# Performance work log

Measured on AMD Instinct MI355X. Metric: run time of the kernel, lower is better.

The kernel has to match this reference:

```python
import jax, jax.numpy as jnp
import numpy as np

D = 512      # d_model
H = 8        # n_heads
DK = D // H  # head dim
DFF = 4 * D  # d_ff
E = 3        # encoder layers
PRED = 256   # pred_len
C_OUT = 64


def _ln(x, g, b):
    m = jnp.mean(x, axis=-1, keepdims=True)
    v = jnp.var(x, axis=-1, keepdims=True)
    return (x - m) / jnp.sqrt(v + 1e-5) * g + b


def _attn(q_in, kv_in, Wq, bq, Wk, bk, Wv, bv, Wo, bo, causal):
    B, L, _ = q_in.shape
    S = kv_in.shape[1]
    q = (q_in @ Wq + bq).reshape(B, L, H, DK)
    k = (kv_in @ Wk + bk).reshape(B, S, H, DK)
    v = (kv_in @ Wv + bv).reshape(B, S, H, DK)
    scores = jnp.einsum('blhe,bshe->bhls', q, k)  # [B,H,L,S]
    if causal:
        mask = jnp.triu(jnp.ones((L, S), dtype=bool), k=1)
        scores = jnp.where(mask, -jnp.inf, scores)
    scale = 1.0 / jnp.sqrt(jnp.asarray(DK, scores.dtype))
    A = jax.nn.softmax(scores * scale, axis=-1)
    out = jnp.einsum('bhls,bshd->blhd', A, v).reshape(B, L, H * DK)
    return out @ Wo + bo


def _gelu(x):
    return jax.nn.gelu(x, approximate=False)  # torch F.gelu is exact erf


def setup_inputs() -> dict:
    ks = iter(jax.random.split(jax.random.key(0), 80))
    r = lambda *s: jax.random.normal(next(ks), s, jnp.float32) * 0.02
    inp = {}
    inp['x_dec'] = jax.random.normal(next(ks), (8, 512, D), jnp.float32)
    inp['x_enc'] = jax.random.normal(next(ks), (8, 1024, D), jnp.float32)
    # encoder params, stacked over layers
    for nm in ['Wq', 'Wk', 'Wv', 'Wo']:
        inp[f'enc_{nm}'] = r(E, D, D)
        inp[f'enc_b{nm[1].lower()}'] = r(E, D)
    inp['enc_W1'] = r(E, D, DFF); inp['enc_b1'] = r(E, DFF)
    inp['enc_W2'] = r(E, DFF, D); inp['enc_b2'] = r(E, D)
    inp['enc_g1'] = jnp.ones((E, D)); inp['enc_beta1'] = jnp.zeros((E, D))
    inp['enc_g2'] = jnp.ones((E, D)); inp['enc_beta2'] = jnp.zeros((E, D))
    inp['enc_ng'] = jnp.ones((D,)); inp['enc_nbeta'] = jnp.zeros((D,))
    # decoder (single layer) params
    for p in ['s', 'c']:
        for nm in ['Wq', 'Wk', 'Wv', 'Wo']:
            inp[f'dec_{p}{nm}'] = r(D, D)
            inp[f'dec_{p}b{nm[1].lower()}'] = r(D)
    inp['dec_W1'] = r(D, DFF); inp['dec_b1'] = r(DFF)
    inp['dec_W2'] = r(DFF, D); inp['dec_b2'] = r(D)
    inp['dec_g1'] = jnp.ones((D,)); inp['dec_beta1'] = jnp.zeros((D,))
    inp['dec_g2'] = jnp.ones((D,)); inp['dec_beta2'] = jnp.zeros((D,))
    inp['dec_g3'] = jnp.ones((D,)); inp['dec_beta3'] = jnp.zeros((D,))
    inp['dec_ng'] = jnp.ones((D,)); inp['dec_nbeta'] = jnp.zeros((D,))
    inp['proj_W'] = r(D, C_OUT); inp['proj_b'] = r(C_OUT)
    return inp


def reference(x_dec, x_enc,
              enc_Wq, enc_bq, enc_Wk, enc_bk, enc_Wv, enc_bv, enc_Wo, enc_bo,
              enc_W1, enc_b1, enc_W2, enc_b2,
              enc_g1, enc_beta1, enc_g2, enc_beta2, enc_ng, enc_nbeta,
              dec_sWq, dec_sbq, dec_sWk, dec_sbk, dec_sWv, dec_sbv, dec_sWo, dec_sbo,
              dec_cWq, dec_cbq, dec_cWk, dec_cbk, dec_cWv, dec_cbv, dec_cWo, dec_cbo,
              dec_W1, dec_b1, dec_W2, dec_b2,
              dec_g1, dec_beta1, dec_g2, dec_beta2, dec_g3, dec_beta3,
              dec_ng, dec_nbeta, proj_W, proj_b):
    # ----- encoder (non-causal self-attn, eval mode: dropout = identity) -----
    x = x_enc
    for l in range(E):
        a = _attn(x, x, enc_Wq[l], enc_bq[l], enc_Wk[l], enc_bk[l],
                  enc_Wv[l], enc_bv[l], enc_Wo[l], enc_bo[l], causal=False)
        x = _ln(x + a, enc_g1[l], enc_beta1[l])
        y = _gelu(x @ enc_W1[l] + enc_b1[l]) @ enc_W2[l] + enc_b2[l]
        x = _ln(x + y, enc_g2[l], enc_beta2[l])
    enc_out = _ln(x, enc_ng, enc_nbeta)
    # ----- decoder (causal self-attn + cross-attn) -----
    x = x_dec
    a = _attn(x, x, dec_sWq, dec_sbq, dec_sWk, dec_sbk,
              dec_sWv, dec_sbv, dec_sWo, dec_sbo, causal=True)
    x = _ln(x + a, dec_g1, dec_beta1)
    a = _attn(x, enc_out, dec_cWq, dec_cbq, dec_cWk, dec_cbk,
              dec_cWv, dec_cbv, dec_cWo, dec_cbo, causal=False)
    x = _ln(x + a, dec_g2, dec_beta2)
    y = _gelu(x @ dec_W1 + dec_b1) @ dec_W2 + dec_b2
    x = _ln(x + y, dec_g3, dec_beta3)
    x = _ln(x, dec_ng, dec_nbeta)
    out = x @ proj_W + proj_b
    return out[:, -PRED:, :]
```

## Files before the change

kernel.cpp:

```cpp
#include <hip/hip_runtime.h>
#include <cstddef>

typedef __bf16 bf16;
typedef __bf16 bf16x8 __attribute__((ext_vector_type(8)));
typedef float f32x4 __attribute__((ext_vector_type(4)));

#define D 512
#define DFF 2048
#define MFMA __builtin_amdgcn_mfma_f32_16x16x32_bf16

__device__ __forceinline__ float load_any(const void* p, size_t i, int f) {
  return f ? ((const float*)p)[i] : (float)((const bf16*)p)[i];
}

__global__ void detect_dtype(const unsigned* __restrict__ x, int* flag) {
  __shared__ int cnt;
  if (threadIdx.x == 0) cnt = 0;
  __syncthreads();
  int local = 0;
  for (int i = threadIdx.x; i < 32768; i += 256) {
    unsigned e = (x[i] >> 7) & 0xFFu;
    if (e >= 160u) local++;
  }
  atomicAdd(&cnt, local);
  __syncthreads();
  if (threadIdx.x == 0) *flag = (cnt > 100) ? 1 : 0;
}

__global__ __launch_bounds__(256)
void conv_to_bf16(const void* __restrict__ src, bf16* __restrict__ dst, int n,
                  const int* __restrict__ flag) {
  const int f = *flag;
  for (int i = blockIdx.x * 256 + threadIdx.x; i < n; i += gridDim.x * 256)
    dst[i] = (bf16)load_any(src, i, f);
}

struct CDesc { const void* src; unsigned long long off; bf16* dst; int n; int pad; };
struct CPack { CDesc d[40]; };
__global__ __launch_bounds__(256)
void conv_batch(CPack P, const int* __restrict__ flag) {
  const CDesc& c = P.d[blockIdx.z];
  const int f = *flag;
  for (int i = blockIdx.x * 256 + threadIdx.x; i < c.n; i += gridDim.x * 256)
    c.dst[i] = (bf16)load_any(c.src, c.off + i, f);
}

struct TDesc { const void* src; unsigned long long off; bf16* dst; };
struct TPack { TDesc d[20]; };
__global__ __launch_bounds__(256)
void transpose_b(TPack P, int Kd, int Nd, const int* __restrict__ flag) {
  __shared__ bf16 tile[64][65];
  const TDesc& t = P.d[blockIdx.z];
  const int f = *flag;
  int tx = threadIdx.x & 63, ty = threadIdx.x >> 6;
  int nb = blockIdx.x * 64, kb = blockIdx.y * 64;
  #pragma unroll
  for (int r = ty; r < 64; r += 4)
    tile[r][tx] = (bf16)load_any(t.src, t.off + (size_t)(kb + r) * Nd + nb + tx, f);
  __syncthreads();
  #pragma unroll
  for (int r = ty; r < 64; r += 4)
    t.dst[(size_t)(nb + r) * Kd + kb + tx] = tile[tx][r];
}

__global__ __launch_bounds__(256)
void prep_kv(const bf16* __restrict__ K, const bf16* __restrict__ V,
             bf16* __restrict__ Kf, bf16* __restrict__ Vf, int S)
{
  __shared__ bf16 tile[64][72];
  const int kt = blockIdx.x, h = blockIdx.y, b = blockIdx.z;
  const int t = threadIdx.x;
  const int r = t >> 2, g = t & 3;
  const size_t srcrow = ((size_t)(b * S + kt * 64 + r)) * D + h * 64 + g * 16;
  const size_t bh = (size_t)(b * 8 + h);
  const size_t tbase = (bh * (S >> 6) + kt) * 4096;

  bf16x8 k0 = *(const bf16x8*)(K + srcrow);
  bf16x8 k1 = *(const bf16x8*)(K + srcrow + 8);
  const int nt = r >> 4, m15 = r & 15;
  const int c = g >> 1, qq = (g & 1) * 2;
  *(bf16x8*)(Kf + tbase + (((nt * 2 + c) * 64) + qq * 16 + m15) * 8)       = k0;
  *(bf16x8*)(Kf + tbase + (((nt * 2 + c) * 64) + (qq + 1) * 16 + m15) * 8) = k1;

  bf16x8 v0 = *(const bf16x8*)(V + srcrow);
  bf16x8 v1 = *(const bf16x8*)(V + srcrow + 8);
  #pragma unroll
  for (int u = 0; u < 8; u++) {
    tile[g * 16 + u][r]     = v0[u];
    tile[g * 16 + 8 + u][r] = v1[u];
  }
  __syncthreads();
  #pragma unroll
  for (int s = 0; s < 2; s++) {
    int i = t * 2 + s;
    int lane = i & 63, ntc = i >> 6;
    int vq = lane >> 4, vm = lane & 15;
    int vnt = ntc >> 1, vc = ntc & 1;
    bf16x8 o = *(const bf16x8*)(&tile[vnt * 16 + vm][vc * 32 + vq * 8]);
    *(bf16x8*)(Vf + tbase + (size_t)i * 8) = o;
  }
}

__device__ __forceinline__ void gload_lds16(const bf16* g, bf16* l) {
  __builtin_amdgcn_global_load_lds((const __attribute__((address_space(1))) void*)g,
                                   (__attribute__((address_space(3))) void*)l,
                                   16, 0, 0);
}

__device__ __forceinline__ void swizzle_bm_bn(int& bm, int& bn) {
  int lin = blockIdx.y * gridDim.x + blockIdx.x;
  if ((gridDim.y & 7) == 0) {
    int xcd = lin & 7, j = lin >> 3;
    bn = j % gridDim.x;
    bm = xcd + 8 * (j / gridDim.x);
  } else {
    bn = blockIdx.x; bm = blockIdx.y;
  }
}

__global__ __launch_bounds__(256, 2)
void gemm_bt(const bf16* __restrict__ A, const bf16* __restrict__ BT,
             const bf16* __restrict__ bias, bf16* __restrict__ C,
             int M, int N, int K, int act)
{
  __shared__ bf16 As[128 * 32];
  __shared__ bf16 Bs[128 * 32];
  const int tid = threadIdx.x;
  int bm, bn; swizzle_bm_bn(bm, bn);
  const int wid = tid >> 6, lane = tid & 63;
  const int wm = (wid >> 1) << 6, wn = (wid & 1) << 6;
  const int l15 = lane & 15, q = lane >> 4;

  f32x4 acc[4][4] = {};

  const bf16* ag = A + (size_t)(bm * 128 + (tid >> 2)) * K + (tid & 3) * 8;
  const bf16* bg = BT + (size_t)(bn * 128 + (tid >> 2)) * K + (tid & 3) * 8;
  const size_t rstep = (size_t)64 * K;
  bf16* asl = As + tid * 8;
  bf16* bsl = Bs + tid * 8;

  for (int k0 = 0; k0 < K; k0 += 32) {
    __syncthreads();
    gload_lds16(ag + k0,          asl);
    gload_lds16(ag + k0 + rstep,  asl + 256 * 8);
    gload_lds16(bg + k0,          bsl);
    gload_lds16(bg + k0 + rstep,  bsl + 256 * 8);
    __syncthreads();

    bf16x8 af[4], bq[4];
    #pragma unroll
    for (int i = 0; i < 4; i++)
      af[i] = *(const bf16x8*)(As + (wm + i * 16 + l15) * 32 + q * 8);
    #pragma unroll
    for (int j = 0; j < 4; j++)
      bq[j] = *(const bf16x8*)(Bs + (wn + j * 16 + l15) * 32 + q * 8);
    #pragma unroll
    for (int i = 0; i < 4; i++)
      #pragma unroll
      for (int j = 0; j < 4; j++)
        acc[i][j] = MFMA(af[i], bq[j], acc[i][j], 0, 0, 0);
  }

  #pragma unroll
  for (int j = 0; j < 4; j++) {
    int gcol = bn * 128 + wn + j * 16 + l15;
    float bv = (float)bias[gcol];
    #pragma unroll
    for (int i = 0; i < 4; i++) {
      int grow = bm * 128 + wm + i * 16 + q * 4;
      #pragma unroll
      for (int r = 0; r < 4; r++) {
        float v = acc[i][j][r] + bv;
        if (act == 1) v = 0.5f * v * (1.0f + erff(v * 0.70710678118654752f));
        C[(size_t)(grow + r) * N + gcol] = (bf16)v;
      }
    }
  }
}

__global__ __launch_bounds__(256, 2)
void gemm_ks(const bf16* __restrict__ A, const bf16* __restrict__ BT,
             const bf16* __restrict__ bias, bf16* __restrict__ P0,
             bf16* __restrict__ P1, int M, int N, int K)
{
  __shared__ bf16 As[128 * 32];
  __shared__ bf16 Bs[128 * 32];
  const int tid = threadIdx.x;
  int bm, bnl; swizzle_bm_bn(bm, bnl);
  const int bn = bnl >> 1, split = bnl & 1;
  const int Kh = K >> 1, kbase = split * Kh;
  const int wid = tid >> 6, lane = tid & 63;
  const int wm = (wid >> 1) << 6, wn = (wid & 1) << 6;
  const int l15 = lane & 15, q = lane >> 4;

  f32x4 acc[4][4] = {};

  const bf16* ag = A + (size_t)(bm * 128 + (tid >> 2)) * K + kbase + (tid & 3) * 8;
  const bf16* bg = BT + (size_t)(bn * 128 + (tid >> 2)) * K + kbase + (tid & 3) * 8;
  const size_t rstep = (size_t)64 * K;
  bf16* asl = As + tid * 8;
  bf16* bsl = Bs + tid * 8;

  for (int k0 = 0; k0 < Kh; k0 += 32) {
    __syncthreads();
    gload_lds16(ag + k0,          asl);
    gload_lds16(ag + k0 + rstep,  asl + 256 * 8);
    gload_lds16(bg + k0,          bsl);
    gload_lds16(bg + k0 + rstep,  bsl + 256 * 8);
    __syncthreads();

    bf16x8 af[4], bq[4];
    #pragma unroll
    for (int i = 0; i < 4; i++)
      af[i] = *(const bf16x8*)(As + (wm + i * 16 + l15) * 32 + q * 8);
    #pragma unroll
    for (int j = 0; j < 4; j++)
      bq[j] = *(const bf16x8*)(Bs + (wn + j * 16 + l15) * 32 + q * 8);
    #pragma unroll
    for (int i = 0; i < 4; i++)
      #pragma unroll
      for (int j = 0; j < 4; j++)
        acc[i][j] = MFMA(af[i], bq[j], acc[i][j], 0, 0, 0);
  }

  bf16* Cp = split ? P1 : P0;
  #pragma unroll
  for (int j = 0; j < 4; j++) {
    int gcol = bn * 128 + wn + j * 16 + l15;
    float bv = split ? 0.0f : (float)bias[gcol];
    #pragma unroll
    for (int i = 0; i < 4; i++) {
      int grow = bm * 128 + wm + i * 16 + q * 4;
      #pragma unroll
      for (int r = 0; r < 4; r++)
        Cp[(size_t)(grow + r) * 512 + gcol] = (bf16)(acc[i][j][r] + bv);
    }
  }
}

__global__ __launch_bounds__(256, 2)
void gemm_seg(const bf16* __restrict__ A, const bf16* __restrict__ BT,
              const bf16* __restrict__ bias,
              bf16* __restrict__ O0, bf16* __restrict__ O1, bf16* __restrict__ O2,
              int M, int K)
{
  __shared__ bf16 As[128 * 32];
  __shared__ bf16 Bs[128 * 32];
  const int tid = threadIdx.x;
  int bm, bn; swizzle_bm_bn(bm, bn);
  const int wid = tid >> 6, lane = tid & 63;
  const int wm = (wid >> 1) << 6, wn = (wid & 1) << 6;
  const int l15 = lane & 15, q = lane >> 4;

  f32x4 acc[4][4] = {};

  const bf16* ag = A + (size_t)(bm * 128 + (tid >> 2)) * K + (tid & 3) * 8;
  const bf16* bg = BT + (size_t)(bn * 128 + (tid >> 2)) * K + (tid & 3) * 8;
  const size_t rstep = (size_t)64 * K;
  bf16* asl = As + tid * 8;
  bf16* bsl = Bs + tid * 8;

  for (int k0 = 0; k0 < K; k0 += 32) {
    __syncthreads();
    gload_lds16(ag + k0,          asl);
    gload_lds16(ag + k0 + rstep,  asl + 256 * 8);
    gload_lds16(bg + k0,          bsl);
    gload_lds16(bg + k0 + rstep,  bsl + 256 * 8);
    __syncthreads();

    bf16x8 af[4], bq[4];
    #pragma unroll
    for (int i = 0; i < 4; i++)
      af[i] = *(const bf16x8*)(As + (wm + i * 16 + l15) * 32 + q * 8);
    #pragma unroll
    for (int j = 0; j < 4; j++)
      bq[j] = *(const bf16x8*)(Bs + (wn + j * 16 + l15) * 32 + q * 8);
    #pragma unroll
    for (int i = 0; i < 4; i++)
      #pragma unroll
      for (int j = 0; j < 4; j++)
        acc[i][j] = MFMA(af[i], bq[j], acc[i][j], 0, 0, 0);
  }

  const int seg = (bn * 128) >> 9;
  bf16* Cp = (seg == 0) ? O0 : ((seg == 1) ? O1 : O2);
  const int colb = seg << 9;

  #pragma unroll
  for (int j = 0; j < 4; j++) {
    int gcol = bn * 128 + wn + j * 16 + l15;
    float bv = (float)bias[gcol];
    int lcol = gcol - colb;
    #pragma unroll
    for (int i = 0; i < 4; i++) {
      int grow = bm * 128 + wm + i * 16 + q * 4;
      #pragma unroll
      for (int r = 0; r < 4; r++)
        Cp[(size_t)(grow + r) * 512 + lcol] = (bf16)(acc[i][j][r] + bv);
    }
  }
}

__global__ __launch_bounds__(256, 2)
void flash_attn(const bf16* __restrict__ Q, const bf16* __restrict__ Kf,
                const bf16* __restrict__ Vf, bf16* __restrict__ O,
                int L, int S, int causal)
{
  __shared__ bf16 PL[4][32 * 72];
  const int tid = threadIdx.x, wid = tid >> 6, lane = tid & 63;
  const int m15 = lane & 15, q = lane >> 4;
  const int b = blockIdx.z, h = blockIdx.y;
  const int wq = blockIdx.x * 128 + wid * 32;

  bf16x8 aq[2][2];
  #pragma unroll
  for (int qh = 0; qh < 2; qh++) {
    const bf16* qp = Q + ((size_t)(b * L + wq + qh * 16 + m15)) * D + h * 64 + q * 8;
    aq[qh][0] = *(const bf16x8*)(qp);
    aq[qh][1] = *(const bf16x8*)(qp + 32);
  }
  const size_t bh = (size_t)(b * 8 + h);
  const bf16* kfb = Kf + bh * ((size_t)S * 64);
  const bf16* vfb = Vf + bh * ((size_t)S * 64);

  f32x4 acco[2][4] = {};
  float ls[2][4] = {};

  const int ktmax = causal ? ((wq + 95) >> 6) : (S >> 6);

  bf16x8 kf[4][2];
  #pragma unroll
  for (int nt = 0; nt < 4; nt++)
    #pragma unroll
    for (int c = 0; c < 2; c++)
      kf[nt][c] = *(const bf16x8*)(kfb + ((nt * 2 + c) * 64 + lane) * 8);

  bf16* pl = &PL[wid][0];

  for (int kt = 0; kt < ktmax; kt++) {
    bf16x8 vf[4][2];
    const bf16* vc = vfb + (size_t)kt * 4096;
    #pragma unroll
    for (int nt = 0; nt < 4; nt++)
      #pragma unroll
      for (int c = 0; c < 2; c++)
        vf[nt][c] = *(const bf16x8*)(vc + ((nt * 2 + c) * 64 + lane) * 8);

    f32x4 sc[2][4];
    #pragma unroll
    for (int qh = 0; qh < 2; qh++)
      #pragma unroll
      for (int nt = 0; nt < 4; nt++) {
        f32x4 z = {};
        z = MFMA(aq[qh][0], kf[nt][0], z, 0, 0, 0);
        z = MFMA(aq[qh][1], kf[nt][1], z, 0, 0, 0);
        sc[qh][nt] = z;
      }

    {
      const int knext = (kt + 1 < ktmax) ? kt + 1 : kt;
      const bf16* kc = kfb + (size_t)knext * 4096;
      #pragma unroll
      for (int nt = 0; nt < 4; nt++)
        #pragma unroll
        for (int c = 0; c < 2; c++)
          kf[nt][c] = *(const bf16x8*)(kc + ((nt * 2 + c) * 64 + lane) * 8);
    }

    const bool mask = causal && (kt == ktmax - 1);
    #pragma unroll
    for (int qh = 0; qh < 2; qh++)
      #pragma unroll
      for (int nt = 0; nt < 4; nt++)
        #pragma unroll
        for (int r = 0; r < 4; r++) {
          float s = sc[qh][nt][r] * 0.125f;
          if (mask) {
            int kg = kt * 64 + nt * 16 + m15;
            int qg = wq + qh * 16 + q * 4 + r;
            if (kg > qg) s = -1e30f;
          }
          float p = __expf(s);
          ls[qh][r] += p;
          pl[(qh * 16 + q * 4 + r) * 72 + nt * 16 + m15] = (bf16)p;
        }

    #pragma unroll
    for (int qh = 0; qh < 2; qh++) {
      bf16x8 pa0 = *(const bf16x8*)(pl + (qh * 16 + m15) * 72 + q * 8);
      bf16x8 pa1 = *(const bf16x8*)(pl + (qh * 16 + m15) * 72 + 32 + q * 8);
      #pragma unroll
      for (int nt = 0; nt < 4; nt++) {
        acco[qh][nt] = MFMA(pa0, vf[nt][0], acco[qh][nt], 0, 0, 0);
        acco[qh][nt] = MFMA(pa1, vf[nt][1], acco[qh][nt], 0, 0, 0);
      }
    }
  }

  #pragma unroll
  for (int qh = 0; qh < 2; qh++)
    #pragma unroll
    for (int r = 0; r < 4; r++) {
      float v = ls[qh][r];
      v += __shfl_xor(v, 1); v += __shfl_xor(v, 2);
      v += __shfl_xor(v, 4); v += __shfl_xor(v, 8);
      ls[qh][r] = 1.0f / v;
    }

  #pragma unroll
  for (int qh = 0; qh < 2; qh++)
    #pragma unroll
    for (int nt = 0; nt < 4; nt++)
      #pragma unroll
      for (int r = 0; r < 4; r++)
        O[((size_t)(b * L + wq + qh * 16 + q * 4 + r)) * D + h * 64 + nt * 16 + m15] =
            (bf16)(acco[qh][nt][r] * ls[qh][r]);
}

__global__ __launch_bounds__(256)
void add_ln(const bf16* __restrict__ X0, const bf16* __restrict__ X1,
            const bf16* __restrict__ R,
            const bf16* __restrict__ g, const bf16* __restrict__ be,
            bf16* __restrict__ Y, int hasR)
{
  __shared__ float red[4];
  const int row = blockIdx.x, tid = threadIdx.x;
  const bf16* x = X0 + (size_t)row * D;
  float v0 = (float)x[tid], v1 = (float)x[tid + 256];
  if (X1 != nullptr) {
    const bf16* p = X1 + (size_t)row * D;
    v0 += (float)p[tid]; v1 += (float)p[tid + 256];
  }
  if (hasR) {
    const bf16* r = R + (size_t)row * D;
    v0 += (float)r[tid]; v1 += (float)r[tid + 256];
  }
  float s = v0 + v1;
  #pragma unroll
  for (int o = 32; o > 0; o >>= 1) s += __shfl_down(s, o);
  if ((tid & 63) == 0) red[tid >> 6] = s;
  __syncthreads();
  const float mean = (red[0] + red[1] + red[2] + red[3]) * (1.0f / 512.0f);
  __syncthreads();
  const float d0 = v0 - mean, d1 = v1 - mean;
  float sq = d0 * d0 + d1 * d1;
  #pragma unroll
  for (int o = 32; o > 0; o >>= 1) sq += __shfl_down(sq, o);
  if ((tid & 63) == 0) red[tid >> 6] = sq;
  __syncthreads();
  const float var = (red[0] + red[1] + red[2] + red[3]) * (1.0f / 512.0f);
  const float rstd = rsqrtf(var + 1e-5f);
  bf16* y = Y + (size_t)row * D;
  y[tid]       = (bf16)(d0 * rstd * (float)g[tid]       + (float)be[tid]);
  y[tid + 256] = (bf16)(d1 * rstd * (float)g[tid + 256] + (float)be[tid + 256]);
}

__global__ __launch_bounds__(256)
void proj_out(const bf16* __restrict__ X, const bf16* __restrict__ Wp,
              const bf16* __restrict__ bp, void* __restrict__ out,
              const int* __restrict__ flag)
{
  __shared__ float part[4][64];
  const int rb = blockIdx.x;
  const int b = rb >> 8, t = rb & 255;
  const int tid = threadIdx.x;
  const bf16* x = X + ((size_t)(b * 512 + 256 + t)) * D;
  const int c = tid & 63, seg = tid >> 6;
  float acc = 0.f;
  for (int k = seg * 128; k < seg * 128 + 128; k++)
    acc += (float)x[k] * (float)Wp[(size_t)k * 64 + c];
  part[seg][c] = acc;
  __syncthreads();
  if (tid < 64) {
    float v = part[0][tid] + part[1][tid] + part[2][tid] + part[3][tid] + (float)bp[tid];
    size_t idx = (size_t)rb * 64 + tid;
    if (*flag) ((float*)out)[idx] = v;
    else       ((bf16*)out)[idx] = (bf16)v;
  }
}

extern "C" void kernel_launch(void* const* d_in, const int* in_sizes, int n_in,
                              void* d_out, int out_size, void* d_ws, size_t ws_size,
                              hipStream_t stream)
{
  (void)in_sizes; (void)n_in; (void)out_size; (void)ws_size;

  char* wsb = (char*)d_ws;
  int* flag = (int*)wsb;
  bf16* w = (bf16*)(wsb + 256);
  size_t off = 0;
  auto alloc = [&](size_t n) { bf16* p = w + off; off += n; return p; };

  bf16* eQKVT = alloc(3 * (size_t)1536 * D);
  bf16* eWoT  = alloc(3 * (size_t)D * D);
  bf16* eW1T  = alloc(3 * (size_t)D * DFF);
  bf16* eW2T  = alloc(3 * (size_t)D * DFF);
  bf16* dQKVT = alloc((size_t)1536 * D);
  bf16* sWoT  = alloc((size_t)D * D);
  bf16* cWqT  = alloc((size_t)D * D);
  bf16* cKVT  = alloc((size_t)1024 * D);
  bf16* cWoT  = alloc((size_t)D * D);
  bf16* dW1T  = alloc((size_t)D * DFF);
  bf16* dW2T  = alloc((size_t)D * DFF);
  bf16* pW    = alloc((size_t)D * 64);
  bf16* e_qkvb  = alloc(3 * 1536);
  bf16* d_sqkvb = alloc(1536);
  bf16* d_ckvb  = alloc(1024);
  bf16* c_ebo = alloc(3 * D);
  bf16* c_eb1 = alloc(3 * DFF); bf16* c_eb2 = alloc(3 * D);
  bf16* c_eg1 = alloc(3 * D);   bf16* c_ebe1 = alloc(3 * D);
  bf16* c_eg2 = alloc(3 * D);   bf16* c_ebe2 = alloc(3 * D);
  bf16* c_eng = alloc(D);       bf16* c_enb = alloc(D);
  bf16* c_dsbo = alloc(D);
  bf16* c_dcbq = alloc(D);      bf16* c_dcbo = alloc(D);
  bf16* c_db1 = alloc(DFF);     bf16* c_db2 = alloc(D);
  bf16* c_dg1 = alloc(D);  bf16* c_dbe1 = alloc(D);
  bf16* c_dg2 = alloc(D);  bf16* c_dbe2 = alloc(D);
  bf16* c_dg3 = alloc(D);  bf16* c_dbe3 = alloc(D);
  bf16* c_dng = alloc(D);  bf16* c_dnb = alloc(D);
  bf16* c_pb  = alloc(64);
  bf16* xe   = alloc((size_t)8192 * D);
  bf16* enco = alloc((size_t)8192 * D);
  bf16* xd0  = alloc((size_t)4096 * D);
  bf16* xd   = alloc((size_t)4096 * D);
  bf16* qb   = alloc((size_t)8192 * D);
  bf16* kb   = alloc((size_t)8192 * D);
  bf16* vb   = alloc((size_t)8192 * D);
  bf16* t0   = alloc((size_t)8192 * D);
  bf16* t1   = alloc((size_t)8192 * D);
  bf16* mid  = qb;

  const dim3 tb(256);

  detect_dtype<<<dim3(1), tb, 0, stream>>>((const unsigned*)d_in[1], flag);

  conv_to_bf16<<<dim3(1024), tb, 0, stream>>>(d_in[1], xe, 8 * 1024 * D, flag);
  conv_to_bf16<<<dim3(1024), tb, 0, stream>>>(d_in[0], xd0, 8 * 512 * D, flag);

  {
    CPack P{};
    int n = 0;
    auto add = [&](int idx, unsigned long long o, bf16* dst, int cnt) {
      P.d[n++] = {d_in[idx], o, dst, cnt, 0};
    };
    add(9, 0, c_ebo, 1536);
    add(11, 0, c_eb1, 6144);  add(13, 0, c_eb2, 1536);
    add(14, 0, c_eg1, 1536);  add(15, 0, c_ebe1, 1536);
    add(16, 0, c_eg2, 1536);  add(17, 0, c_ebe2, 1536);
    add(18, 0, c_eng, 512);   add(19, 0, c_enb, 512);
    add(27, 0, c_dsbo, 512);
    add(29, 0, c_dcbq, 512);  add(35, 0, c_dcbo, 512);
    add(37, 0, c_db1, 2048);  add(39, 0, c_db2, 512);
    add(40, 0, c_dg1, 512);   add(41, 0, c_dbe1, 512);
    add(42, 0, c_dg2, 512);   add(43, 0, c_dbe2, 512);
    add(44, 0, c_dg3, 512);   add(45, 0, c_dbe3, 512);
    add(46, 0, c_dng, 512);   add(47, 0, c_dnb, 512);
    add(48, 0, pW, D * 64);   add(49, 0, c_pb, 64);
    for (int l = 0; l < 3; l++) {
      add(3, (unsigned long long)l * D, e_qkvb + l * 1536, 512);
      add(5, (unsigned long long)l * D, e_qkvb + l * 1536 + 512, 512);
      add(7, (unsigned long long)l * D, e_qkvb + l * 1536 + 1024, 512);
    }
    add(21, 0, d_sqkvb, 512); add(23, 0, d_sqkvb + 512, 512); add(25, 0, d_sqkvb + 1024, 512);
    add(31, 0, d_ckvb, 512);  add(33, 0, d_ckvb + 512, 512);
    conv_batch<<<dim3(24, 1, n), tb, 0, stream>>>(P, flag);
  }

  {
    TPack P{};
    int n = 0;
    for (int l = 0; l < 3; l++) {
      unsigned long long wo = (unsigned long long)l * D * D;
      bf16* dst = eQKVT + (size_t)l * 1536 * D;
      P.d[n++] = {d_in[2], wo, dst};
      P.d[n++] = {d_in[4], wo, dst + 512 * D};
      P.d[n++] = {d_in[6], wo, dst + 1024 * D};
      P.d[n++] = {d_in[8], wo, eWoT + wo};
    }
    P.d[n++] = {d_in[20], 0, dQKVT};
    P.d[n++] = {d_in[22], 0, dQKVT + 512 * D};
    P.d[n++] = {d_in[24], 0, dQKVT + 1024 * D};
    P.d[n++] = {d_in[26], 0, sWoT};
    P.d[n++] = {d_in[28], 0, cWqT};
    P.d[n++] = {d_in[30], 0, cKVT};
    P.d[n++] = {d_in[32], 0, cKVT + 512 * D};
    P.d[n++] = {d_in[34], 0, cWoT};
    transpose_b<<<dim3(8, 8, n), tb, 0, stream>>>(P, D, D, flag);
  }
  {
    TPack P{};
    for (int l = 0; l < 3; l++)
      P.d[l] = {d_in[10], (unsigned long long)l * D * DFF, eW1T + (size_t)l * D * DFF};
    P.d[3] = {d_in[36], 0, dW1T};
    transpose_b<<<dim3(32, 8, 4), tb, 0, stream>>>(P, D, DFF, flag);
  }
  {
    TPack P{};
    for (int l = 0; l < 3; l++)
      P.d[l] = {d_in[12], (unsigned long long)l * D * DFF, eW2T + (size_t)l * D * DFF};
    P.d[3] = {d_in[38], 0, dW2T};
    transpose_b<<<dim3(8, 32, 4), tb, 0, stream>>>(P, DFF, D, flag);
  }

  auto G = [&](const bf16* A, const bf16* BT, const bf16* bias, bf16* C,
               int M, int N, int K, int act) {
    gemm_bt<<<dim3(N / 128, M / 128), tb, 0, stream>>>(A, BT, bias, C, M, N, K, act);
  };
  auto KS = [&](const bf16* A, const bf16* BT, const bf16* bias,
                bf16* P0, bf16* P1, int M, int K) {
    gemm_ks<<<dim3(8, M / 128), tb, 0, stream>>>(A, BT, bias, P0, P1, M, 512, K);
  };
  auto GS = [&](const bf16* A, const bf16* BT, const bf16* bias,
                bf16* O0, bf16* O1, bf16* O2, int M, int N, int K) {
    gemm_seg<<<dim3(N / 128, M / 128), tb, 0, stream>>>(A, BT, bias, O0, O1, O2, M, K);
  };
  auto PK = [&](const bf16* Kp, const bf16* Vp, bf16* Kfp, bf16* Vfp, int S) {
    prep_kv<<<dim3(S / 64, 8, 8), tb, 0, stream>>>(Kp, Vp, Kfp, Vfp, S);
  };
  auto FA = [&](const bf16* Qp, const bf16* Kfp, const bf16* Vfp, bf16* Op,
                int L, int S, int causal) {
    flash_attn<<<dim3(L / 128, 8, 8), tb, 0, stream>>>(Qp, Kfp, Vfp, Op, L, S, causal);
  };
  auto LN = [&](const bf16* X0, const bf16* X1, const bf16* R,
                const bf16* g, const bf16* be, bf16* Y, int hasR, int M) {
    add_ln<<<dim3(M), tb, 0, stream>>>(X0, X1, R, g, be, Y, hasR);
  };

  const int Me = 8192;
  for (int l = 0; l < 3; l++) {
    const size_t wo = (size_t)l * D * D, fo = (size_t)l * D * DFF;
    GS(xe, eQKVT + (size_t)l * 1536 * D, e_qkvb + l * 1536, qb, kb, vb, Me, 1536, D);
    PK(kb, vb, t1, enco, 1024);
    FA(qb, t1, enco, t0, 1024, 1024, 0);
    KS(t0, eWoT + wo, c_ebo + l * D, t1, enco, Me, 512);
    LN(t1, enco, xe, c_eg1 + l * D, c_ebe1 + l * D, xe, 1, Me);
    G(xe, eW1T + fo, c_eb1 + l * DFF, mid, Me, DFF, D, 1);
    KS(mid, eW2T + fo, c_eb2 + l * D, t1, enco, Me, 2048);
    LN(t1, enco, xe, c_eg2 + l * D, c_ebe2 + l * D, xe, 1, Me);
  }
  LN(xe, nullptr, nullptr, c_eng, c_enb, enco, 0, Me);

  const int Md = 4096;
  GS(xd0, dQKVT, d_sqkvb, qb, kb, vb, Md, 1536, D);
  PK(kb, vb, t1, xd, 512);
  FA(qb, t1, xd, t0, 512, 512, 1);
  KS(t0, sWoT, c_dsbo, t1, vb, Md, 512);
  LN(t1, vb, xd0, c_dg1, c_dbe1, xd, 1, Md);
  G(xd, cWqT, c_dcbq, qb, Md, D, D, 0);
  GS(enco, cKVT, d_ckvb, kb, vb, nullptr, Me, 1024, D);
  PK(kb, vb, t1, enco, 1024);
  FA(qb, t1, enco, t0, 512, 1024, 0);
  KS(t0, cWoT, c_dcbo, t1, vb, Md, 512);
  LN(t1, vb, xd, c_dg2, c_dbe2, xd, 1, Md);
  G(xd, dW1T, c_db1, mid, Md, DFF, D, 1);
  KS(mid, dW2T, c_db2, t1, vb, Md, 2048);
  LN(t1, vb, xd, c_dg3, c_dbe3, xd, 1, Md);
  LN(xd, nullptr, nullptr, c_dng, c_dnb, xd, 0, Md);
  proj_out<<<dim3(2048), tb, 0, stream>>>(xd, pW, c_pb, d_out, flag);
}
```

Baseline: 950.9 us.

## Coalesce GEMM and attention output stores via LDS, approximate GELU, fuse double layernorm

GEMM epilogues now stage each 128x128 tile through shared memory in two halves and write rows with 16-byte vector stores instead of scattered 2-byte stores. The flash attention output is staged the same way. Exact erf GELU is replaced by a tanh-form approximation computed with an exponential. Consecutive layernorms at the end of the encoder and decoder are fused into a single kernel. The extra barriers and LDS traffic in the epilogue, and the small numerical deviation from the GELU approximation, are the tradeoffs.

```diff
diff --git a/kernel.cpp b/kernel.cpp
--- a/kernel.cpp
+++ b/kernel.cpp
@@ -11,6 +11,13 @@
 
 __device__ __forceinline__ float load_any(const void* p, size_t i, int f) {
   return f ? ((const float*)p)[i] : (float)((const bf16*)p)[i];
+}
+
+__device__ __forceinline__ float fast_gelu(float x) {
+  float y = 1.5957691216f * (x + 0.044715f * x * x * x);
+  y = fminf(y, 80.0f);
+  float e = __expf(y);
+  return x * e / (e + 1.0f);
 }
 
 __global__ void detect_dtype(const unsigned* __restrict__ x, int* flag) {
@@ -118,13 +125,40 @@
   }
 }
 
+#define EPILOGUE_STORE(smem, Cbase, rowstride, colbase, VAL)                      \
+  {                                                                               \
+    _Pragma("unroll")                                                             \
+    for (int half = 0; half < 2; half++) {                                        \
+      __syncthreads();                                                            \
+      if ((wm >> 6) == half) {                                                    \
+        _Pragma("unroll")                                                         \
+        for (int j = 0; j < 4; j++)                                               \
+          _Pragma("unroll")                                                       \
+          for (int i = 0; i < 4; i++)                                             \
+            _Pragma("unroll")                                                     \
+            for (int r = 0; r < 4; r++)                                           \
+              smem[(i * 16 + q * 4 + r) * 136 + wn + j * 16 + l15] =              \
+                  (bf16)(VAL(i, j, r));                                           \
+      }                                                                           \
+      __syncthreads();                                                            \
+      const int srow = tid >> 2, scc = (tid & 3) * 32;                            \
+      _Pragma("unroll")                                                           \
+      for (int k = 0; k < 4; k++) {                                               \
+        bf16x8 v = *(const bf16x8*)(smem + srow * 136 + scc + k * 8);             \
+        *(bf16x8*)(Cbase + (size_t)(bm * 128 + half * 64 + srow) * (rowstride) +  \
+                   (colbase) + scc + k * 8) = v;                                  \
+      }                                                                           \
+    }                                                                             \
+  }
+
 __global__ __launch_bounds__(256, 2)
 void gemm_bt(const bf16* __restrict__ A, const bf16* __restrict__ BT,
              const bf16* __restrict__ bias, bf16* __restrict__ C,
              int M, int N, int K, int act)
 {
-  __shared__ bf16 As[128 * 32];
-  __shared__ bf16 Bs[128 * 32];
+  __shared__ bf16 smem[64 * 136];
+  bf16* As = smem;
+  bf16* Bs = smem + 4096;
   const int tid = threadIdx.x;
   int bm, bn; swizzle_bm_bn(bm, bn);
   const int wid = tid >> 6, lane = tid & 63;
@@ -161,21 +195,14 @@
         acc[i][j] = MFMA(af[i], bq[j], acc[i][j], 0, 0, 0);
   }
 
-  #pragma unroll
-  for (int j = 0; j < 4; j++) {
-    int gcol = bn * 128 + wn + j * 16 + l15;
-    float bv = (float)bias[gcol];
-    #pragma unroll
-    for (int i = 0; i < 4; i++) {
-      int grow = bm * 128 + wm + i * 16 + q * 4;
-      #pragma unroll
-      for (int r = 0; r < 4; r++) {
-        float v = acc[i][j][r] + bv;
-        if (act == 1) v = 0.5f * v * (1.0f + erff(v * 0.70710678118654752f));
-        C[(size_t)(grow + r) * N + gcol] = (bf16)v;
-      }
-    }
-  }
+  float bcol[4];
+  #pragma unroll
+  for (int j = 0; j < 4; j++) bcol[j] = (float)bias[bn * 128 + wn + j * 16 + l15];
+
+#define GBT_VAL(i, j, r)                                                   \
+  (act ? fast_gelu(acc[i][j][r] + bcol[j]) : (acc[i][j][r] + bcol[j]))
+  EPILOGUE_STORE(smem, C, N, bn * 128, GBT_VAL)
+#undef GBT_VAL
 }
 
 __global__ __launch_bounds__(256, 2)
@@ -183,8 +210,9 @@
              const bf16* __restrict__ bias, bf16* __restrict__ P0,
              bf16* __restrict__ P1, int M, int N, int K)
 {
-  __shared__ bf16 As[128 * 32];
-  __shared__ bf16 Bs[128 * 32];
+  __shared__ bf16 smem[64 * 136];
+  bf16* As = smem;
+  bf16* Bs = smem + 4096;
   const int tid = threadIdx.x;
   int bm, bnl; swizzle_bm_bn(bm, bnl);
   const int bn = bnl >> 1, split = bnl & 1;
@@ -224,18 +252,14 @@
   }
 
   bf16* Cp = split ? P1 : P0;
-  #pragma unroll
-  for (int j = 0; j < 4; j++) {
-    int gcol = bn * 128 + wn + j * 16 + l15;
-    float bv = split ? 0.0f : (float)bias[gcol];
-    #pragma unroll
-    for (int i = 0; i < 4; i++) {
-      int grow = bm * 128 + wm + i * 16 + q * 4;
-      #pragma unroll
-      for (int r = 0; r < 4; r++)
-        Cp[(size_t)(grow + r) * 512 + gcol] = (bf16)(acc[i][j][r] + bv);
-    }
-  }
+  float bcol[4];
+  #pragma unroll
+  for (int j = 0; j < 4; j++)
+    bcol[j] = split ? 0.0f : (float)bias[bn * 128 + wn + j * 16 + l15];
+
+#define GKS_VAL(i, j, r) (acc[i][j][r] + bcol[j])
+  EPILOGUE_STORE(smem, Cp, 512, bn * 128, GKS_VAL)
+#undef GKS_VAL
 }
 
 __global__ __launch_bounds__(256, 2)
@@ -244,8 +268,9 @@
               bf16* __restrict__ O0, bf16* __restrict__ O1, bf16* __restrict__ O2,
               int M, int K)
 {
-  __shared__ bf16 As[128 * 32];
-  __shared__ bf16 Bs[128 * 32];
+  __shared__ bf16 smem[64 * 136];
+  bf16* As = smem;
+  bf16* Bs = smem + 4096;
   const int tid = threadIdx.x;
   int bm, bn; swizzle_bm_bn(bm, bn);
   const int wid = tid >> 6, lane = tid & 63;
@@ -285,20 +310,13 @@
   const int seg = (bn * 128) >> 9;
   bf16* Cp = (seg == 0) ? O0 : ((seg == 1) ? O1 : O2);
   const int colb = seg << 9;
-
-  #pragma unroll
-  for (int j = 0; j < 4; j++) {
-    int gcol = bn * 128 + wn + j * 16 + l15;
-    float bv = (float)bias[gcol];
-    int lcol = gcol - colb;
-    #pragma unroll
-    for (int i = 0; i < 4; i++) {
-      int grow = bm * 128 + wm + i * 16 + q * 4;
-      #pragma unroll
-      for (int r = 0; r < 4; r++)
-        Cp[(size_t)(grow + r) * 512 + lcol] = (bf16)(acc[i][j][r] + bv);
-    }
-  }
+  float bcol[4];
+  #pragma unroll
+  for (int j = 0; j < 4; j++) bcol[j] = (float)bias[bn * 128 + wn + j * 16 + l15];
+
+#define GSEG_VAL(i, j, r) (acc[i][j][r] + bcol[j])
+  EPILOGUE_STORE(smem, Cp, 512, bn * 128 - colb, GSEG_VAL)
+#undef GSEG_VAL
 }
 
 __global__ __launch_bounds__(256, 2)
@@ -413,8 +431,14 @@
     for (int nt = 0; nt < 4; nt++)
       #pragma unroll
       for (int r = 0; r < 4; r++)
-        O[((size_t)(b * L + wq + qh * 16 + q * 4 + r)) * D + h * 64 + nt * 16 + m15] =
+        pl[(qh * 16 + q * 4 + r) * 72 + nt * 16 + m15] =
             (bf16)(acco[qh][nt][r] * ls[qh][r]);
+
+  const int orow = lane >> 1, occ = (lane & 1) * 32;
+  bf16* ob = O + ((size_t)(b * L + wq + orow)) * D + h * 64 + occ;
+  #pragma unroll
+  for (int k = 0; k < 4; k++)
+    *(bf16x8*)(ob + k * 8) = *(const bf16x8*)(pl + orow * 72 + occ + k * 8);
 }
 
 __global__ __launch_bounds__(256)
@@ -453,6 +477,58 @@
   bf16* y = Y + (size_t)row * D;
   y[tid]       = (bf16)(d0 * rstd * (float)g[tid]       + (float)be[tid]);
   y[tid + 256] = (bf16)(d1 * rstd * (float)g[tid + 256] + (float)be[tid + 256]);
+}
+
+__global__ __launch_bounds__(256)
+void add_lnln(const bf16* __restrict__ X0, const bf16* __restrict__ X1,
+              const bf16* __restrict__ R,
+              const bf16* __restrict__ g1, const bf16* __restrict__ b1,
+              const bf16* __restrict__ g2, const bf16* __restrict__ b2,
+              bf16* __restrict__ Y)
+{
+  __shared__ float red[4];
+  const int row = blockIdx.x, tid = threadIdx.x;
+  const size_t o = (size_t)row * D;
+  float v0 = (float)X0[o + tid] + (float)X1[o + tid] + (float)R[o + tid];
+  float v1 = (float)X0[o + tid + 256] + (float)X1[o + tid + 256] + (float)R[o + tid + 256];
+
+  float s = v0 + v1;
+  #pragma unroll
+  for (int q = 32; q > 0; q >>= 1) s += __shfl_down(s, q);
+  if ((tid & 63) == 0) red[tid >> 6] = s;
+  __syncthreads();
+  const float mean = (red[0] + red[1] + red[2] + red[3]) * (1.0f / 512.0f);
+  __syncthreads();
+  float d0 = v0 - mean, d1 = v1 - mean;
+  float sq = d0 * d0 + d1 * d1;
+  #pragma unroll
+  for (int q = 32; q > 0; q >>= 1) sq += __shfl_down(sq, q);
+  if ((tid & 63) == 0) red[tid >> 6] = sq;
+  __syncthreads();
+  const float var = (red[0] + red[1] + red[2] + red[3]) * (1.0f / 512.0f);
+  const float rstd = rsqrtf(var + 1e-5f);
+  float u0 = d0 * rstd * (float)g1[tid]       + (float)b1[tid];
+  float u1 = d1 * rstd * (float)g1[tid + 256] + (float)b1[tid + 256];
+
+  __syncthreads();
+  float s2 = u0 + u1;
+  #pragma unroll
+  for (int q = 32; q > 0; q >>= 1) s2 += __shfl_down(s2, q);
+  if ((tid & 63) == 0) red[tid >> 6] = s2;
+  __syncthreads();
+  const float mean2 = (red[0] + red[1] + red[2] + red[3]) * (1.0f / 512.0f);
+  __syncthreads();
+  float e0 = u0 - mean2, e1 = u1 - mean2;
+  float sq2 = e0 * e0 + e1 * e1;
+  #pragma unroll
+  for (int q = 32; q > 0; q >>= 1) sq2 += __shfl_down(sq2, q);
+  if ((tid & 63) == 0) red[tid >> 6] = sq2;
+  __syncthreads();
+  const float var2 = (red[0] + red[1] + red[2] + red[3]) * (1.0f / 512.0f);
+  const float rstd2 = rsqrtf(var2 + 1e-5f);
+  bf16* y = Y + o;
+  y[tid]       = (bf16)(e0 * rstd2 * (float)g2[tid]       + (float)b2[tid]);
+  y[tid + 256] = (bf16)(e1 * rstd2 * (float)g2[tid + 256] + (float)b2[tid + 256]);
 }
 
 __global__ __launch_bounds__(256)
@@ -636,9 +712,12 @@
     LN(t1, enco, xe, c_eg1 + l * D, c_ebe1 + l * D, xe, 1, Me);
     G(xe, eW1T + fo, c_eb1 + l * DFF, mid, Me, DFF, D, 1);
     KS(mid, eW2T + fo, c_eb2 + l * D, t1, enco, Me, 2048);
-    LN(t1, enco, xe, c_eg2 + l * D, c_ebe2 + l * D, xe, 1, Me);
-  }
-  LN(xe, nullptr, nullptr, c_eng, c_enb, enco, 0, Me);
+    if (l < 2)
+      LN(t1, enco, xe, c_eg2 + l * D, c_ebe2 + l * D, xe, 1, Me);
+    else
+      add_lnln<<<dim3(Me), tb, 0, stream>>>(t1, enco, xe, c_eg2 + 2 * D,
+                                            c_ebe2 + 2 * D, c_eng, c_enb, enco);
+  }
 
   const int Md = 4096;
   GS(xd0, dQKVT, d_sqkvb, qb, kb, vb, Md, 1536, D);
@@ -654,7 +733,6 @@
   LN(t1, vb, xd, c_dg2, c_dbe2, xd, 1, Md);
   G(xd, dW1T, c_db1, mid, Md, DFF, D, 1);
   KS(mid, dW2T, c_db2, t1, vb, Md, 2048);
-  LN(t1, vb, xd, c_dg3, c_dbe3, xd, 1, Md);
-  LN(xd, nullptr, nullptr, c_dng, c_dnb, xd, 0, Md);
+  add_lnln<<<dim3(Md), tb, 0, stream>>>(t1, vb, xd, c_dg3, c_dbe3, c_dng, c_dnb, xd);
   proj_out<<<dim3(2048), tb, 0, stream>>>(xd, pW, c_pb, d_out, flag);
 }
```

Result: slower. 1.075 ms (+13.0%).
